# Performance work log

Measured on AMD Instinct MI355X. Metric: run time of the kernel, lower is better.

Reference implementation:

```python
import jax, jax.numpy as jnp
import numpy as np

N = 262144   # nodes
H = 256      # hidden_dim
NH = 8       # num_heads
HD = H // NH # head_dim = 32
C = 100      # num_commits
L = 2        # transformer layers


def _layer_norm(x, g, b, eps=1e-5):
    mu = jnp.mean(x, axis=-1, keepdims=True)
    var = jnp.mean(jnp.square(x - mu), axis=-1, keepdims=True)
    return (x - mu) * jax.lax.rsqrt(var + eps) * g + b


def setup_inputs() -> dict:
    key = jax.random.key(0)
    ks = jax.random.split(key, 16)
    w = lambda k, shape: jax.random.normal(k, shape, jnp.float32) * 0.02
    inp = {
        "node_embeddings": jax.random.normal(ks[0], (N, H), jnp.float32),
        "commit_indices": jax.random.randint(ks[1], (N,), 0, C),
        "num_commits": C,
        "commit_queries": jax.random.normal(ks[2], (NH, HD), jnp.float32),
        "k_w": w(ks[3], (H, H)), "k_b": jnp.zeros(H, jnp.float32),
        "v_w": w(ks[4], (H, H)), "v_b": jnp.zeros(H, jnp.float32),
        "po_w": w(ks[5], (H, H)), "po_b": jnp.zeros(H, jnp.float32),
        "pn_g": jnp.ones(H, jnp.float32), "pn_b": jnp.zeros(H, jnp.float32),
        "t_in_w": w(ks[6], (L, 3 * H, H)), "t_in_b": jnp.zeros((L, 3 * H), jnp.float32),
        "t_out_w": w(ks[7], (L, H, H)), "t_out_b": jnp.zeros((L, H), jnp.float32),
        "t_ln1_g": jnp.ones((L, H), jnp.float32), "t_ln1_b": jnp.zeros((L, H), jnp.float32),
        "t_ff1_w": w(ks[8], (L, 4 * H, H)), "t_ff1_b": jnp.zeros((L, 4 * H), jnp.float32),
        "t_ff2_w": w(ks[9], (L, H, 4 * H)), "t_ff2_b": jnp.zeros((L, H), jnp.float32),
        "t_ln2_g": jnp.ones((L, H), jnp.float32), "t_ln2_b": jnp.zeros((L, H), jnp.float32),
        "r1_w": w(ks[10], (H // 2, H)), "r1_b": jnp.zeros(H // 2, jnp.float32),
        "r2_w": w(ks[11], (1, H // 2)), "r2_b": jnp.zeros(1, jnp.float32),
    }
    return inp


def reference(node_embeddings, commit_indices, num_commits, commit_queries,
              k_w, k_b, v_w, v_b, po_w, po_b, pn_g, pn_b,
              t_in_w, t_in_b, t_out_w, t_out_b, t_ln1_g, t_ln1_b,
              t_ff1_w, t_ff1_b, t_ff2_w, t_ff2_b, t_ln2_g, t_ln2_b,
              r1_w, r1_b, r2_w, r2_b):
    nh, hd = commit_queries.shape
    scale = hd ** -0.5
    n = node_embeddings.shape[0]
    seg = commit_indices

    # --- segmented multi-head attention pooling (replaces per-commit loop) ---
    K = (node_embeddings @ k_w.T + k_b).reshape(n, nh, hd)   # [N,H,D]
    V = (node_embeddings @ v_w.T + v_b).reshape(n, nh, hd)
    scores = jnp.einsum('hd,nhd->nh', commit_queries, K) * scale  # [N,H]
    m = jax.ops.segment_max(scores, seg, num_segments=num_commits)  # [C,H]
    m = jnp.where(jnp.isfinite(m), m, 0.0)                          # empty commits
    e = jnp.exp(scores - m[seg])                                    # [N,H]
    den = jax.ops.segment_sum(e, seg, num_segments=num_commits)     # [C,H]
    num = jax.ops.segment_sum(e[:, :, None] * V, seg, num_segments=num_commits)  # [C,H,D]
    pooled = num / jnp.where(den > 0, den, 1.0)[:, :, None]
    counts = jax.ops.segment_sum(jnp.ones((n,), node_embeddings.dtype), seg,
                                 num_segments=num_commits)
    emb = _layer_norm(pooled.reshape(num_commits, nh * hd) @ po_w.T + po_b, pn_g, pn_b)
    x = jnp.where((counts > 0)[:, None], emb, 0.0)                  # [C,hidden]

    # --- commit transformer (seq len = C, batch = 1, post-norm, gelu) ---
    for l in range(t_in_w.shape[0]):
        qkv = x @ t_in_w[l].T + t_in_b[l]
        q, k, v = jnp.split(qkv, 3, axis=-1)
        q = q.reshape(num_commits, nh, hd)
        k = k.reshape(num_commits, nh, hd)
        v = v.reshape(num_commits, nh, hd)
        a = jax.nn.softmax(jnp.einsum('nhd,mhd->hnm', q, k) * scale, axis=-1)
        o = jnp.einsum('hnm,mhd->nhd', a, v).reshape(num_commits, nh * hd)
        o = o @ t_out_w[l].T + t_out_b[l]
        x = _layer_norm(x + o, t_ln1_g[l], t_ln1_b[l])
        ff = jax.nn.gelu(x @ t_ff1_w[l].T + t_ff1_b[l], approximate=False)
        ff = ff @ t_ff2_w[l].T + t_ff2_b[l]
        x = _layer_norm(x + ff, t_ln2_g[l], t_ln2_b[l])

    # --- ranking head ---
    h = jax.nn.gelu(x @ r1_w.T + r1_b, approximate=False)
    return (h @ r2_w.T + r2_b).squeeze(-1)  # [C]
```

## Files before the change

### kernel.cpp

```cpp
#include <hip/hip_runtime.h>
#include <math.h>

#define NNODES 262144
#define HDIM   256
#define NHEADS 8
#define HEADD  32
#define NC     100
#define NLAYER 2
#define SPLIT  16
#define NBLK   (NNODES/256)

__device__ __forceinline__ float gelu_exact(float v) {
    return 0.5f * v * (1.0f + erff(v * 0.70710678118654752440f));
}

__device__ __forceinline__ float dot4(float4 a, float4 b) {
    return a.x*b.x + a.y*b.y + a.z*b.z + a.w*b.w;
}

__device__ __forceinline__ float blk_sum256(float v, float* red, int tid) {
    #pragma unroll
    for (int m = 32; m >= 1; m >>= 1) v += __shfl_xor(v, m, 64);
    if ((tid & 63) == 0) red[tid >> 6] = v;
    __syncthreads();
    float tot = red[0] + red[1] + red[2] + red[3];
    __syncthreads();
    return tot;
}

__global__ void k_qkw(const float* __restrict__ q, const float* __restrict__ kw,
                      const float* __restrict__ kb, float* __restrict__ qk_w,
                      float* __restrict__ qk_b) {
    int h = blockIdx.x, j = threadIdx.x;
    float s = 0.f;
    #pragma unroll
    for (int d = 0; d < HEADD; ++d) s += q[h*HEADD + d] * kw[(h*HEADD + d)*HDIM + j];
    qk_w[h*HDIM + j] = s;
    if (j == 0) {
        float sb = 0.f;
        #pragma unroll
        for (int d = 0; d < HEADD; ++d) sb += q[h*HEADD + d] * kb[h*HEADD + d];
        qk_b[h] = sb;
    }
}

__global__ __launch_bounds__(256) void k_hist(const int* __restrict__ cidx,
                                              int* __restrict__ hist) {
    __shared__ int l_hist[NC];
    int tid = threadIdx.x;
    for (int i = tid; i < NC; i += 256) l_hist[i] = 0;
    __syncthreads();
    int c = cidx[blockIdx.x * 256 + tid];
    atomicAdd(&l_hist[c], 1);
    __syncthreads();
    for (int i = tid; i < NC; i += 256) hist[blockIdx.x*NC + i] = l_hist[i];
}

__global__ __launch_bounds__(256) void k_blockscan(const int* __restrict__ hist,
        int* __restrict__ bbase, int* __restrict__ counts) {
    int c = blockIdx.x, t = threadIdx.x;
    int v[4]; int loc = 0;
    #pragma unroll
    for (int i = 0; i < 4; ++i) { v[i] = hist[(t*4 + i)*NC + c]; loc += v[i]; }
    __shared__ int sc[256];
    sc[t] = loc; __syncthreads();
    for (int off = 1; off < 256; off <<= 1) {
        int x = (t >= off) ? sc[t - off] : 0;
        __syncthreads();
        sc[t] += x;
        __syncthreads();
    }
    int run = (t > 0) ? sc[t-1] : 0;
    #pragma unroll
    for (int i = 0; i < 4; ++i) { bbase[(t*4 + i)*NC + c] = run; run += v[i]; }
    if (t == 255) counts[c] = sc[255];
}

__global__ void k_scan(const int* __restrict__ counts, int* __restrict__ offs) {
    if (threadIdx.x == 0) {
        int o = 0;
        for (int c = 0; c < NC; ++c) { offs[c] = o; o += counts[c]; }
        offs[NC] = o;
    }
}

__global__ __launch_bounds__(256) void k_scatter(const int* __restrict__ cidx,
        const int* __restrict__ offs, const int* __restrict__ bbase,
        int* __restrict__ nlist) {
    __shared__ int sb[NC];
    __shared__ int lcur[NC];
    int t = threadIdx.x, blk = blockIdx.x;
    if (t < NC) { sb[t] = offs[t] + bbase[blk*NC + t]; lcur[t] = 0; }
    __syncthreads();
    int n = blk * 256 + t;
    int c = cidx[n];
    int p = atomicAdd(&lcur[c], 1);
    nlist[sb[c] + p] = n;
}

__global__ __launch_bounds__(256) void k_accum(const float* __restrict__ emb,
        const int* __restrict__ nlist, const int* __restrict__ offs,
        const int* __restrict__ counts, const float* __restrict__ qk_w,
        const float* __restrict__ qk_b, float* __restrict__ S_part,
        float* __restrict__ den_part) {
    int c  = blockIdx.x / SPLIT;
    int sl = blockIdx.x % SPLIT;
    int cnt = counts[c];
    __shared__ float s_buf[2][NHEADS*HDIM];
    __shared__ float s_den[2][NHEADS];
    int tid = threadIdx.x, w = tid >> 6, lane = tid & 63;
    int s = lane & 7, i = lane >> 3;
    const float scale = 0.17677669529663688f;

    float4 w4[NHEADS];
    #pragma unroll
    for (int h = 0; h < NHEADS; ++h)
        w4[h] = ((const float4*)(qk_w + h*HDIM))[lane];
    float qkb_s = qk_b[s];

    float4 acc[NHEADS];
    #pragma unroll
    for (int h = 0; h < NHEADS; ++h) acc[h] = make_float4(0.f, 0.f, 0.f, 0.f);
    float den_l = 0.f;

    int beg = offs[c];
    int per = (cnt + SPLIT - 1) / SPLIT;
    int s0 = min(cnt, sl * per), s1 = min(cnt, s0 + per);

    for (int base = s0 + w*8; base < s1; base += 32) {
        int nb = min(8, s1 - base);
        int nn = (i < nb) ? nlist[beg + base + i] : 0;
        float4 e4buf[8];
        #pragma unroll
        for (int i2 = 0; i2 < 8; ++i2) {
            if (i2 < nb) {
                int n2 = __shfl(nn, i2*8, 64);
                e4buf[i2] = ((const float4*)(emb + (size_t)n2 * HDIM))[lane];
            }
        }
        #pragma unroll
        for (int i2 = 0; i2 < 8; ++i2) {
            if (i2 >= nb) break;
            float4 e4 = e4buf[i2];
            float p[NHEADS];
            #pragma unroll
            for (int h = 0; h < NHEADS; ++h) p[h] = dot4(e4, w4[h]);
            float q0, q1, q2, q3;
            {
                bool sel = (s & 1) != 0;
                float a0 = __shfl_xor(p[0], 1, 64), a1 = __shfl_xor(p[1], 1, 64);
                q0 = sel ? (p[1] + a1) : (p[0] + a0);
                float a2 = __shfl_xor(p[2], 1, 64), a3 = __shfl_xor(p[3], 1, 64);
                q1 = sel ? (p[3] + a3) : (p[2] + a2);
                float a4 = __shfl_xor(p[4], 1, 64), a5 = __shfl_xor(p[5], 1, 64);
                q2 = sel ? (p[5] + a5) : (p[4] + a4);
                float a6 = __shfl_xor(p[6], 1, 64), a7 = __shfl_xor(p[7], 1, 64);
                q3 = sel ? (p[7] + a7) : (p[6] + a6);
            }
            float r0, r1;
            {
                bool sel = (s & 2) != 0;
                float b0 = __shfl_xor(q0, 2, 64), b1 = __shfl_xor(q1, 2, 64);
                r0 = sel ? (q1 + b1) : (q0 + b0);
                float b2 = __shfl_xor(q2, 2, 64), b3 = __shfl_xor(q3, 2, 64);
                r1 = sel ? (q3 + b3) : (q2 + b2);
            }
            float tt;
            {
                bool sel = (s & 4) != 0;
                float c0 = __shfl_xor(r0, 4, 64), c1 = __shfl_xor(r1, 4, 64);
                tt = sel ? (r1 + c1) : (r0 + c0);
            }
            tt += __shfl_xor(tt, 8, 64);
            tt += __shfl_xor(tt, 16, 64);
            tt += __shfl_xor(tt, 32, 64);
            float ev = __expf((tt + qkb_s) * scale);
            den_l += ev;
            #pragma unroll
            for (int h2 = 0; h2 < NHEADS; ++h2) {
                float ee = __shfl(ev, h2, 64);
                acc[h2].x += ee * e4.x; acc[h2].y += ee * e4.y;
                acc[h2].z += ee * e4.z; acc[h2].w += ee * e4.w;
            }
        }
    }
    if (w >= 2) {
        #pragma unroll
        for (int h2 = 0; h2 < NHEADS; ++h2)
            ((float4*)&s_buf[w-2][h2*HDIM])[lane] = acc[h2];
        if (lane < NHEADS) s_den[w-2][lane] = den_l;
    }
    __syncthreads();
    if (w < 2) {
        #pragma unroll
        for (int h2 = 0; h2 < NHEADS; ++h2) {
            float4 v = ((const float4*)&s_buf[w][h2*HDIM])[lane];
            acc[h2].x += v.x; acc[h2].y += v.y; acc[h2].z += v.z; acc[h2].w += v.w;
        }
        if (lane < NHEADS) den_l += s_den[w][lane];
    }
    __syncthreads();
    if (w == 1) {
        #pragma unroll
        for (int h2 = 0; h2 < NHEADS; ++h2)
            ((float4*)&s_buf[0][h2*HDIM])[lane] = acc[h2];
        if (lane < NHEADS) s_den[0][lane] = den_l;
    }
    __syncthreads();
    if (w == 0) {
        float* Sd = S_part + ((size_t)sl*NC + c) * (NHEADS*HDIM);
        #pragma unroll
        for (int h2 = 0; h2 < NHEADS; ++h2) {
            float4 v = ((const float4*)&s_buf[0][h2*HDIM])[lane];
            v.x += acc[h2].x; v.y += acc[h2].y; v.z += acc[h2].z; v.w += acc[h2].w;
            ((float4*)(Sd + h2*HDIM))[lane] = v;
        }
        if (lane < NHEADS)
            den_part[(sl*NC + c)*NHEADS + lane] = den_l + s_den[0][lane];
    }
}

__global__ __launch_bounds__(256) void k_pool(const float* __restrict__ S_part,
        const float* __restrict__ den_part, const int* __restrict__ counts,
        const float* __restrict__ vw, const float* __restrict__ vb,
        const float* __restrict__ pow_, const float* __restrict__ pob,
        const float* __restrict__ png, const float* __restrict__ pnb,
        float* __restrict__ x) {
    int c = blockIdx.x, t = threadIdx.x;
    __shared__ float S_l[NHEADS*HDIM];
    __shared__ float pooled[HDIM];
    __shared__ float red[4];
    {
        float4 a0 = make_float4(0.f,0.f,0.f,0.f), a1 = a0;
        #pragma unroll
        for (int sl = 0; sl < SPLIT; ++sl) {
            const float4* sp = (const float4*)(S_part + ((size_t)sl*NC + c) * (NHEADS*HDIM));
            float4 v0 = sp[t], v1 = sp[t + 256];
            a0.x += v0.x; a0.y += v0.y; a0.z += v0.z; a0.w += v0.w;
            a1.x += v1.x; a1.y += v1.y; a1.z += v1.z; a1.w += v1.w;
        }
        ((float4*)S_l)[t] = a0;
        ((float4*)S_l)[t + 256] = a1;
    }
    int h = t >> 5;
    float dh = 0.f;
    #pragma unroll
    for (int sl = 0; sl < SPLIT; ++sl) dh += den_part[(sl*NC + c)*NHEADS + h];
    __syncthreads();
    float dx = dh > 0.f ? dh : 1.f;
    float s = vb[t] * dh;
    const float4* wr = (const float4*)(vw + (size_t)t * HDIM);
    const float4* sr = (const float4*)(S_l + h * HDIM);
    #pragma unroll 8
    for (int j = 0; j < HDIM/4; ++j) s += dot4(wr[j], sr[j]);
    pooled[t] = s / dx;
    __syncthreads();
    float o = pob[t];
    const float4* pr = (const float4*)(pow_ + (size_t)t * HDIM);
    const float4* pv = (const float4*)pooled;
    #pragma unroll 8
    for (int j = 0; j < HDIM/4; ++j) o += dot4(pr[j], pv[j]);
    float mu  = blk_sum256(o, red, t) * (1.f/256.f);
    float d   = o - mu;
    float var = blk_sum256(d*d, red, t) * (1.f/256.f);
    float y = d * rsqrtf(var + 1e-5f) * png[t] + pnb[t];
    x[c*HDIM + t] = (counts[c] > 0) ? y : 0.f;
}

__global__ __launch_bounds__(256) void k_mm(const float* __restrict__ in,
        const float* __restrict__ W, const float* __restrict__ bias,
        float* __restrict__ out, int K, int P, int do_gelu) {
    int r = blockIdx.x;
    int p = blockIdx.y * 256 + threadIdx.x;
    __shared__ float xr[1024];
    for (int idx = threadIdx.x; idx < K; idx += 256) xr[idx] = in[(size_t)r*K + idx];
    __syncthreads();
    float s = bias[p];
    const float4* wr = (const float4*)(W + (size_t)p * K);
    const float4* xv = (const float4*)xr;
    for (int j = 0; j < (K >> 2); ++j) s += dot4(wr[j], xv[j]);
    if (do_gelu) s = gelu_exact(s);
    out[(size_t)r*P + p] = s;
}

__global__ __launch_bounds__(256) void k_mm_res_ln(const float* __restrict__ in,
        const float* __restrict__ W, const float* __restrict__ bias,
        const float* __restrict__ g, const float* __restrict__ be,
        float* __restrict__ x, int K) {
    int r = blockIdx.x, t = threadIdx.x;
    __shared__ float xr[1024];
    __shared__ float red[4];
    for (int idx = t; idx < K; idx += 256) xr[idx] = in[(size_t)r*K + idx];
    __syncthreads();
    float s = bias[t];
    const float4* wr = (const float4*)(W + (size_t)t * K);
    const float4* xv = (const float4*)xr;
    for (int j = 0; j < (K >> 2); ++j) s += dot4(wr[j], xv[j]);
    float v = x[r*HDIM + t] + s;
    float mu  = blk_sum256(v, red, t) * (1.f/256.f);
    float d   = v - mu;
    float var = blk_sum256(d*d, red, t) * (1.f/256.f);
    x[r*HDIM + t] = d * rsqrtf(var + 1e-5f) * g[t] + be[t];
}

__global__ __launch_bounds__(256) void k_attn(const float* __restrict__ qkv,
        float* __restrict__ attn_out) {
    int h = blockIdx.x, t = threadIdx.x;
    __shared__ float k_l[NC * HEADD];
    __shared__ float sc[NC * NC];
    for (int idx = t; idx < NC*HEADD; idx += 256) {
        int n = idx >> 5, d = idx & 31;
        k_l[idx] = qkv[n*768 + 256 + h*HEADD + d];
    }
    __syncthreads();
    const float scale = 0.17677669529663688f;
    for (int idx = t; idx < NC*NC; idx += 256) {
        int n = idx / NC, m = idx - n*NC;
        const float4* q4 = (const float4*)(qkv + n*768 + h*HEADD);
        const float4* k4 = (const float4*)(k_l + m*HEADD);
        float s = 0.f;
        #pragma unroll
        for (int j = 0; j < HEADD/4; ++j) s += dot4(q4[j], k4[j]);
        sc[idx] = s * scale;
    }
    __syncthreads();
    if (t < NC) {
        float mx = -1e30f;
        for (int m = 0; m < NC; ++m) mx = fmaxf(mx, sc[t*NC + m]);
        float sum = 0.f;
        for (int m = 0; m < NC; ++m) { float e = expf(sc[t*NC + m] - mx); sc[t*NC + m] = e; sum += e; }
        float inv = 1.f / sum;
        for (int m = 0; m < NC; ++m) sc[t*NC + m] *= inv;
    }
    __syncthreads();
    for (int idx = t; idx < NC*HEADD; idx += 256) {
        int n = idx >> 5, d = idx & 31;
        float o = 0.f;
        for (int m = 0; m < NC; ++m) o += sc[n*NC + m] * qkv[m*768 + 512 + h*HEADD + d];
        attn_out[n*HDIM + h*HEADD + d] = o;
    }
}

__global__ __launch_bounds__(128) void k_head(const float* __restrict__ x,
        const float* __restrict__ r1w, const float* __restrict__ r1b,
        const float* __restrict__ r2w, const float* __restrict__ r2b,
        float* __restrict__ out) {
    int r = blockIdx.x, t = threadIdx.x;
    __shared__ float xr[HDIM];
    __shared__ float red[2];
    xr[t] = x[r*HDIM + t];
    xr[t + 128] = x[r*HDIM + t + 128];
    __syncthreads();
    float s = r1b[t];
    const float4* wr = (const float4*)(r1w + (size_t)t * HDIM);
    const float4* xv = (const float4*)xr;
    #pragma unroll 8
    for (int j = 0; j < HDIM/4; ++j) s += dot4(wr[j], xv[j]);
    s = gelu_exact(s);
    float contrib = s * r2w[t];
    #pragma unroll
    for (int m = 32; m >= 1; m >>= 1) contrib += __shfl_xor(contrib, m, 64);
    if ((t & 63) == 0) red[t >> 6] = contrib;
    __syncthreads();
    if (t == 0) out[r] = red[0] + red[1] + r2b[0];
}

extern "C" void kernel_launch(void* const* d_in, const int* in_sizes, int n_in,
                              void* d_out, int out_size, void* d_ws, size_t ws_size,
                              hipStream_t stream) {
    const float* emb   = (const float*)d_in[0];
    const int*   cidx  = (const int*)d_in[1];
    const float* q     = (const float*)d_in[3];
    const float* kw    = (const float*)d_in[4];
    const float* kb    = (const float*)d_in[5];
    const float* vw    = (const float*)d_in[6];
    const float* vb    = (const float*)d_in[7];
    const float* pow_  = (const float*)d_in[8];
    const float* pob   = (const float*)d_in[9];
    const float* png   = (const float*)d_in[10];
    const float* pnb   = (const float*)d_in[11];
    const float* tinw  = (const float*)d_in[12];
    const float* tinb  = (const float*)d_in[13];
    const float* toutw = (const float*)d_in[14];
    const float* toutb = (const float*)d_in[15];
    const float* ln1g  = (const float*)d_in[16];
    const float* ln1b  = (const float*)d_in[17];
    const float* ff1w  = (const float*)d_in[18];
    const float* ff1b  = (const float*)d_in[19];
    const float* ff2w  = (const float*)d_in[20];
    const float* ff2b  = (const float*)d_in[21];
    const float* ln2g  = (const float*)d_in[22];
    const float* ln2b  = (const float*)d_in[23];
    const float* r1w   = (const float*)d_in[24];
    const float* r1b   = (const float*)d_in[25];
    const float* r2w   = (const float*)d_in[26];
    const float* r2b   = (const float*)d_in[27];
    float* out = (float*)d_out;

    char* ws = (char*)d_ws;
    size_t off = 0;
    auto alloc = [&](size_t bytes) -> char* {
        off = (off + 255) & ~(size_t)255;
        char* p = ws + off;
        off += bytes;
        return p;
    };
    int*   hist   = (int*)alloc((size_t)NBLK * NC * 4);
    int*   bbase  = (int*)alloc((size_t)NBLK * NC * 4);
    int*   counts = (int*)alloc(NC * 4);
    int*   offs   = (int*)alloc((NC + 1) * 4);
    float* den_p  = (float*)alloc((size_t)SPLIT * NC * NHEADS * 4);
    float* S_part = (float*)alloc((size_t)SPLIT * NC * NHEADS * HDIM * 4);
    float* qk_w   = (float*)alloc(NHEADS * HDIM * 4);
    float* qk_b   = (float*)alloc(NHEADS * 4);
    int*   nlist  = (int*)alloc((size_t)NNODES * 4);
    float* x      = (float*)alloc(NC * HDIM * 4);
    float* qkv    = (float*)alloc(NC * 3 * HDIM * 4);
    float* attn_o = (float*)alloc(NC * HDIM * 4);
    float* ffb    = (float*)alloc(NC * 4 * HDIM * 4);
    (void)ws_size; (void)in_sizes; (void)n_in; (void)out_size;

    k_qkw<<<NHEADS, HDIM, 0, stream>>>(q, kw, kb, qk_w, qk_b);
    k_hist<<<NBLK, 256, 0, stream>>>(cidx, hist);
    k_blockscan<<<NC, 256, 0, stream>>>(hist, bbase, counts);
    k_scan<<<1, 64, 0, stream>>>(counts, offs);
    k_scatter<<<NBLK, 256, 0, stream>>>(cidx, offs, bbase, nlist);
    k_accum<<<NC*SPLIT, 256, 0, stream>>>(emb, nlist, offs, counts, qk_w, qk_b, S_part, den_p);
    k_pool<<<NC, 256, 0, stream>>>(S_part, den_p, counts, vw, vb, pow_, pob, png, pnb, x);

    for (int l = 0; l < NLAYER; ++l) {
        k_mm<<<dim3(NC, 3), 256, 0, stream>>>(x, tinw + (size_t)l*3*HDIM*HDIM,
                                              tinb + (size_t)l*3*HDIM, qkv, HDIM, 3*HDIM, 0);
        k_attn<<<NHEADS, 256, 0, stream>>>(qkv, attn_o);
        k_mm_res_ln<<<NC, 256, 0, stream>>>(attn_o, toutw + (size_t)l*HDIM*HDIM,
                                            toutb + (size_t)l*HDIM, ln1g + (size_t)l*HDIM,
                                            ln1b + (size_t)l*HDIM, x, HDIM);
        k_mm<<<dim3(NC, 4), 256, 0, stream>>>(x, ff1w + (size_t)l*4*HDIM*HDIM,
                                              ff1b + (size_t)l*4*HDIM, ffb, HDIM, 4*HDIM, 1);
        k_mm_res_ln<<<NC, 256, 0, stream>>>(ffb, ff2w + (size_t)l*HDIM*4*HDIM,
                                            ff2b + (size_t)l*HDIM, ln2g + (size_t)l*HDIM,
                                            ln2b + (size_t)l*HDIM, x, 4*HDIM);
    }
    k_head<<<NC, 128, 0, stream>>>(x, r1w, r1b, r2w, r2b, out);
}
```

Before: 798.7 us.

## Split score computation into a streaming kernel before segmented accumulation

Adds a k_score kernel that streams embeddings contiguously, computes per-node per-head exp scores and writes them to a new [N,8] buffer. k_accum then gathers only embeddings plus precomputed scores, keeping a one-row software prefetch instead of an 8-row register buffer, and declares higher occupancy bounds. k_scan becomes a parallel shared-memory scan. The cost is a second full read of the 256 MB embedding matrix plus an extra score buffer, traded for coalesced scoring and a lighter gather loop.

```diff
diff --git a/kernel.cpp b/kernel.cpp
--- a/kernel.cpp
+++ b/kernel.cpp
@@ -44,6 +44,66 @@
     }
 }
 
+__global__ __launch_bounds__(256, 6) void k_score(const float* __restrict__ emb,
+        const float* __restrict__ qk_w, const float* __restrict__ qk_b,
+        float* __restrict__ ev_out) {
+    int tid = threadIdx.x, w = tid >> 6, lane = tid & 63;
+    int s = lane & 7;
+    int gw = blockIdx.x * 4 + w;
+    int r0 = gw * 64;
+    const float scale = 0.17677669529663688f;
+
+    float4 w4[NHEADS];
+    #pragma unroll
+    for (int h = 0; h < NHEADS; ++h)
+        w4[h] = ((const float4*)(qk_w + h*HDIM))[lane];
+    float qkb_s = qk_b[s];
+
+    const float4* base = (const float4*)(emb + (size_t)r0 * HDIM);
+    float4 nxt = base[lane];
+    float keep = 0.f;
+    for (int r = 0; r < 64; ++r) {
+        float4 cur = nxt;
+        if (r < 63) nxt = base[(r + 1) * 64 + lane];
+        float p[NHEADS];
+        #pragma unroll
+        for (int h = 0; h < NHEADS; ++h) p[h] = dot4(cur, w4[h]);
+        float q0, q1, q2, q3;
+        {
+            bool sel = (s & 1) != 0;
+            float a0 = __shfl_xor(p[0], 1, 64), a1 = __shfl_xor(p[1], 1, 64);
+            q0 = sel ? (p[1] + a1) : (p[0] + a0);
+            float a2 = __shfl_xor(p[2], 1, 64), a3 = __shfl_xor(p[3], 1, 64);
+            q1 = sel ? (p[3] + a3) : (p[2] + a2);
+            float a4 = __shfl_xor(p[4], 1, 64), a5 = __shfl_xor(p[5], 1, 64);
+            q2 = sel ? (p[5] + a5) : (p[4] + a4);
+            float a6 = __shfl_xor(p[6], 1, 64), a7 = __shfl_xor(p[7], 1, 64);
+            q3 = sel ? (p[7] + a7) : (p[6] + a6);
+        }
+        float r0v, r1v;
+        {
+            bool sel = (s & 2) != 0;
+            float b0 = __shfl_xor(q0, 2, 64), b1 = __shfl_xor(q1, 2, 64);
+            r0v = sel ? (q1 + b1) : (q0 + b0);
+            float b2 = __shfl_xor(q2, 2, 64), b3 = __shfl_xor(q3, 2, 64);
+            r1v = sel ? (q3 + b3) : (q2 + b2);
+        }
+        float tt;
+        {
+            bool sel = (s & 4) != 0;
+            float c0 = __shfl_xor(r0v, 4, 64), c1 = __shfl_xor(r1v, 4, 64);
+            tt = sel ? (r1v + c1) : (r0v + c0);
+        }
+        tt += __shfl_xor(tt, 8, 64);
+        tt += __shfl_xor(tt, 16, 64);
+        tt += __shfl_xor(tt, 32, 64);
+        float evv = __expf((tt + qkb_s) * scale);
+        if ((lane >> 3) == (r & 7)) keep = evv;
+        if ((r & 7) == 7)
+            ev_out[(size_t)(r0 + r - 7) * NHEADS + lane] = keep;
+    }
+}
+
 __global__ __launch_bounds__(256) void k_hist(const int* __restrict__ cidx,
                                               int* __restrict__ hist) {
     __shared__ int l_hist[NC];
@@ -77,11 +137,17 @@
 }
 
 __global__ void k_scan(const int* __restrict__ counts, int* __restrict__ offs) {
-    if (threadIdx.x == 0) {
-        int o = 0;
-        for (int c = 0; c < NC; ++c) { offs[c] = o; o += counts[c]; }
-        offs[NC] = o;
-    }
+    __shared__ int sc[128];
+    int t = threadIdx.x;
+    int v = (t < NC) ? counts[t] : 0;
+    sc[t] = v; __syncthreads();
+    for (int off = 1; off < 128; off <<= 1) {
+        int x = (t >= off) ? sc[t - off] : 0;
+        __syncthreads();
+        sc[t] += x;
+        __syncthreads();
+    }
+    if (t <= NC) offs[t] = sc[t] - v;
 }
 
 __global__ __launch_bounds__(256) void k_scatter(const int* __restrict__ cidx,
@@ -98,11 +164,10 @@
     nlist[sb[c] + p] = n;
 }
 
-__global__ __launch_bounds__(256) void k_accum(const float* __restrict__ emb,
-        const int* __restrict__ nlist, const int* __restrict__ offs,
-        const int* __restrict__ counts, const float* __restrict__ qk_w,
-        const float* __restrict__ qk_b, float* __restrict__ S_part,
-        float* __restrict__ den_part) {
+__global__ __launch_bounds__(256, 8) void k_accum(const float* __restrict__ emb,
+        const float* __restrict__ ev, const int* __restrict__ nlist,
+        const int* __restrict__ offs, const int* __restrict__ counts,
+        float* __restrict__ S_part, float* __restrict__ den_part) {
     int c  = blockIdx.x / SPLIT;
     int sl = blockIdx.x % SPLIT;
     int cnt = counts[c];
@@ -110,13 +175,6 @@
     __shared__ float s_den[2][NHEADS];
     int tid = threadIdx.x, w = tid >> 6, lane = tid & 63;
     int s = lane & 7, i = lane >> 3;
-    const float scale = 0.17677669529663688f;
-
-    float4 w4[NHEADS];
-    #pragma unroll
-    for (int h = 0; h < NHEADS; ++h)
-        w4[h] = ((const float4*)(qk_w + h*HDIM))[lane];
-    float qkb_s = qk_b[s];
 
     float4 acc[NHEADS];
     #pragma unroll
@@ -130,57 +188,23 @@
     for (int base = s0 + w*8; base < s1; base += 32) {
         int nb = min(8, s1 - base);
         int nn = (i < nb) ? nlist[beg + base + i] : 0;
-        float4 e4buf[8];
-        #pragma unroll
-        for (int i2 = 0; i2 < 8; ++i2) {
-            if (i2 < nb) {
-                int n2 = __shfl(nn, i2*8, 64);
-                e4buf[i2] = ((const float4*)(emb + (size_t)n2 * HDIM))[lane];
+        int n2 = __shfl(nn, 0, 64);
+        float4 e_n = ((const float4*)(emb + (size_t)n2 * HDIM))[lane];
+        float  v_n = ev[(size_t)n2 * NHEADS + s];
+        for (int i2 = 0; i2 < nb; ++i2) {
+            float4 e_c = e_n;
+            float  v_c = v_n;
+            if (i2 + 1 < nb) {
+                int nx = __shfl(nn, (i2 + 1) * 8, 64);
+                e_n = ((const float4*)(emb + (size_t)nx * HDIM))[lane];
+                v_n = ev[(size_t)nx * NHEADS + s];
             }
-        }
-        #pragma unroll
-        for (int i2 = 0; i2 < 8; ++i2) {
-            if (i2 >= nb) break;
-            float4 e4 = e4buf[i2];
-            float p[NHEADS];
-            #pragma unroll
-            for (int h = 0; h < NHEADS; ++h) p[h] = dot4(e4, w4[h]);
-            float q0, q1, q2, q3;
-            {
-                bool sel = (s & 1) != 0;
-                float a0 = __shfl_xor(p[0], 1, 64), a1 = __shfl_xor(p[1], 1, 64);
-                q0 = sel ? (p[1] + a1) : (p[0] + a0);
-                float a2 = __shfl_xor(p[2], 1, 64), a3 = __shfl_xor(p[3], 1, 64);
-                q1 = sel ? (p[3] + a3) : (p[2] + a2);
-                float a4 = __shfl_xor(p[4], 1, 64), a5 = __shfl_xor(p[5], 1, 64);
-                q2 = sel ? (p[5] + a5) : (p[4] + a4);
-                float a6 = __shfl_xor(p[6], 1, 64), a7 = __shfl_xor(p[7], 1, 64);
-                q3 = sel ? (p[7] + a7) : (p[6] + a6);
-            }
-            float r0, r1;
-            {
-                bool sel = (s & 2) != 0;
-                float b0 = __shfl_xor(q0, 2, 64), b1 = __shfl_xor(q1, 2, 64);
-                r0 = sel ? (q1 + b1) : (q0 + b0);
-                float b2 = __shfl_xor(q2, 2, 64), b3 = __shfl_xor(q3, 2, 64);
-                r1 = sel ? (q3 + b3) : (q2 + b2);
-            }
-            float tt;
-            {
-                bool sel = (s & 4) != 0;
-                float c0 = __shfl_xor(r0, 4, 64), c1 = __shfl_xor(r1, 4, 64);
-                tt = sel ? (r1 + c1) : (r0 + c0);
-            }
-            tt += __shfl_xor(tt, 8, 64);
-            tt += __shfl_xor(tt, 16, 64);
-            tt += __shfl_xor(tt, 32, 64);
-            float ev = __expf((tt + qkb_s) * scale);
-            den_l += ev;
+            den_l += v_c;
             #pragma unroll
             for (int h2 = 0; h2 < NHEADS; ++h2) {
-                float ee = __shfl(ev, h2, 64);
-                acc[h2].x += ee * e4.x; acc[h2].y += ee * e4.y;
-                acc[h2].z += ee * e4.z; acc[h2].w += ee * e4.w;
+                float ee = __shfl(v_c, h2, 8);
+                acc[h2].x += ee * e_c.x; acc[h2].y += ee * e_c.y;
+                acc[h2].z += ee * e_c.z; acc[h2].w += ee * e_c.w;
             }
         }
     }
@@ -418,14 +442,16 @@
     float* qkv    = (float*)alloc(NC * 3 * HDIM * 4);
     float* attn_o = (float*)alloc(NC * HDIM * 4);
     float* ffb    = (float*)alloc(NC * 4 * HDIM * 4);
+    float* ev     = (float*)alloc((size_t)NNODES * NHEADS * 4);
     (void)ws_size; (void)in_sizes; (void)n_in; (void)out_size;
 
     k_qkw<<<NHEADS, HDIM, 0, stream>>>(q, kw, kb, qk_w, qk_b);
+    k_score<<<NBLK, 256, 0, stream>>>(emb, qk_w, qk_b, ev);
     k_hist<<<NBLK, 256, 0, stream>>>(cidx, hist);
     k_blockscan<<<NC, 256, 0, stream>>>(hist, bbase, counts);
-    k_scan<<<1, 64, 0, stream>>>(counts, offs);
+    k_scan<<<1, 128, 0, stream>>>(counts, offs);
     k_scatter<<<NBLK, 256, 0, stream>>>(cidx, offs, bbase, nlist);
-    k_accum<<<NC*SPLIT, 256, 0, stream>>>(emb, nlist, offs, counts, qk_w, qk_b, S_part, den_p);
+    k_accum<<<NC*SPLIT, 256, 0, stream>>>(emb, ev, nlist, offs, counts, S_part, den_p);
     k_pool<<<NC, 256, 0, stream>>>(S_part, den_p, counts, vw, vb, pow_, pob, png, pnb, x);
 
     for (int l = 0; l < NLAYER; ++l) {
```

After: 785.0 us. Within noise of the previous version (-1.7%).
